# Optimization experiments

Measured on AMD Instinct MI355X. Metric: run time of the kernel, lower is better.

The kernel has to match this reference:

```python
import jax, jax.numpy as jnp
import numpy as np

TEMP = 0.07
EPS = 1e-6
NORM_EPS = 1e-12  # F.normalize default eps
LN_EPS = 1e-5

B, D, H, W = 32, 256, 64, 64
K = 256
DFF = 2048


def _l2norm(v, axis):
    n = jnp.sqrt(jnp.sum(v * v, axis=axis, keepdims=True))
    return v / jnp.maximum(n, NORM_EPS)


def _layernorm(v, g, b):
    mu = jnp.mean(v, axis=-1, keepdims=True)
    var = jnp.mean((v - mu) ** 2, axis=-1, keepdims=True)
    return (v - mu) * jax.lax.rsqrt(var + LN_EPS) * g + b


def setup_inputs() -> dict:
    key = jax.random.key(0)
    ks = jax.random.split(key, 8)
    s1 = 1.0 / np.sqrt(D)
    s2 = 1.0 / np.sqrt(DFF)
    return {
        "x": jax.random.normal(ks[0], (B, D, H, W), jnp.float32),
        "tgt": jax.random.normal(ks[1], (B, K, D), jnp.float32),
        "w1": jax.random.uniform(ks[2], (DFF, D), jnp.float32, -s1, s1),
        "b1": jax.random.uniform(ks[3], (DFF,), jnp.float32, -s1, s1),
        "w2": jax.random.uniform(ks[4], (D, DFF), jnp.float32, -s2, s2),
        "b2": jax.random.uniform(ks[5], (D,), jnp.float32, -s2, s2),
        "g2": jnp.ones((D,), jnp.float32),
        "be2": jnp.zeros((D,), jnp.float32),
        "g3": jnp.ones((D,), jnp.float32),
        "be3": jnp.zeros((D,), jnp.float32),
    }


def reference(x, tgt, w1, b1, w2, b2, g2, be2, g3, be3):
    # slot cross-attention with L2-normalized q/k
    tn = _l2norm(tgt, axis=2)           # (b,k,d)
    xn = _l2norm(x, axis=1)             # (b,d,h,w)
    dots = jnp.einsum('bkd,bdhw->bkhw', tn, xn)
    attn = jax.nn.softmax(dots / TEMP, axis=1) + EPS          # softmax over slots
    attn = attn / jnp.sum(attn, axis=(2, 3), keepdims=True)   # spatial normalization
    tgt2 = jnp.einsum('bdhw,bkhw->bkd', x, attn)
    t = _layernorm(tgt + tgt2, g2, be2)
    # FFN (dropout = identity in eval)
    ff = jnp.maximum(t @ w1.T + b1, 0.0) @ w2.T + b2
    return _layernorm(t + ff, g3, be3)
```

## Files before the change

kernel.cpp:

```cpp
#include <hip/hip_runtime.h>
#include <hip/hip_bf16.h>

using bf16 = __hip_bfloat16;

typedef __attribute__((ext_vector_type(8))) short short8;
typedef __attribute__((ext_vector_type(4))) float f32x4;

constexpr int Bb = 32, Dd = 256, HWw = 4096, Kk = 256, Ff = 2048;
constexpr float TEMP_INV = 1.0f / 0.07f;
constexpr float EPSf = 1e-6f;
constexpr float NORM_EPSf = 1e-12f;
constexpr float LN_EPSf = 1e-5f;
constexpr size_t PKD = (size_t)Bb * Kk * Dd;

static __device__ __forceinline__ float b2f(bf16 v) { return __bfloat162float(v); }
static __device__ __forceinline__ bf16 f2b(float v) { return __float2bfloat16(v); }


__global__ __launch_bounds__(64) void k_tn(const float* __restrict__ tgt,
                                           bf16* __restrict__ tnbf) {
  int row = blockIdx.x;
  int b = row >> 8, slot = row & 255;
  int lane = threadIdx.x;
  const float* src = tgt + (size_t)row * Dd + lane * 4;
  float v[4];
#pragma unroll
  for (int u = 0; u < 4; u++) v[u] = src[u];
  float ss = v[0] * v[0] + v[1] * v[1] + v[2] * v[2] + v[3] * v[3];
#pragma unroll
  for (int m = 32; m >= 1; m >>= 1) ss += __shfl_xor(ss, m, 64);
  float inv = 1.0f / fmaxf(sqrtf(ss), NORM_EPSf);
  bf16 o[4] __attribute__((aligned(8)));
#pragma unroll
  for (int u = 0; u < 4; u++) o[u] = f2b(v[u] * inv);
  int s = lane >> 3;
  int q2 = (lane >> 1) & 3;
  int jh = (lane & 1) * 4;
  size_t fi = (size_t)((slot >> 4) * 64 + q2 * 16 + (slot & 15));
  *(float2*)(tnbf + ((size_t)(b * 8 + s) * 1024 + fi) * 8 + jh) = *(float2*)o;
}

__global__ __launch_bounds__(64) void k_prew1(const float* __restrict__ w1,
                                              bf16* __restrict__ w1bf) {
  int f = blockIdx.x;
  int lane = threadIdx.x;
  const float* src = w1 + (size_t)f * Dd + lane * 4;
  bf16 o[4] __attribute__((aligned(8)));
#pragma unroll
  for (int u = 0; u < 4; u++) o[u] = f2b(src[u]);
  int s = lane >> 3;
  int q2 = (lane >> 1) & 3;
  int jh = (lane & 1) * 4;
  size_t fi = (size_t)(((f & 63) >> 4) * 64 + q2 * 16 + (f & 15));
  *(float2*)(w1bf + ((size_t)((f >> 6) * 8 + s) * 256 + fi) * 8 + jh) = *(float2*)o;
}

__global__ __launch_bounds__(64) void k_prew2(const float* __restrict__ w2,
                                              bf16* __restrict__ w2bf) {
  int d = blockIdx.x;
  int lane = threadIdx.x;
  const float* src = w2 + (size_t)d * Ff + lane * 32;
  size_t gbase = (size_t)((d >> 6) * 64 + lane) * 256;
  int fbase = ((d & 63) >> 4) * 64 + (d & 15);
#pragma unroll
  for (int q2 = 0; q2 < 4; q2++) {
    float4 v0 = *(const float4*)(src + q2 * 8);
    float4 v1 = *(const float4*)(src + q2 * 8 + 4);
    bf16 o[8] __attribute__((aligned(16)));
    o[0] = f2b(v0.x); o[1] = f2b(v0.y); o[2] = f2b(v0.z); o[3] = f2b(v0.w);
    o[4] = f2b(v1.x); o[5] = f2b(v1.y); o[6] = f2b(v1.z); o[7] = f2b(v1.w);
    *(float4*)(w2bf + (gbase + fbase + q2 * 16) * 8) = *(float4*)o;
  }
}

#define MFMA16(a, b, c) __builtin_amdgcn_mfma_f32_16x16x32_bf16(a, b, c, 0, 0, 0)

__global__ __launch_bounds__(256, 3) void k_dots(const bf16* __restrict__ tnbf,
                                                 const float* __restrict__ x,
                                                 bf16* __restrict__ xb_bf,
                                                 bf16* __restrict__ attn_bf,
                                                 float* __restrict__ S) {
  __shared__ __align__(16) char smem[23296];
  bf16* Bs = (bf16*)smem;
  float* ssred = (float*)(smem + 16640);
  float* nxl = (float*)(smem + 20992);
  float* red = (float*)(smem + 21248);
  int b = blockIdx.x >> 6;
  int hw0 = (blockIdx.x & 63) * 64;
  int tid = threadIdx.x;
  int wave = tid >> 6, lane = tid & 63;
  int quad = lane >> 4, nl = lane & 15;

  int dp = tid >> 4;
  int ch = tid & 15;
  int qb = dp >> 2;
  int jb = (dp & 3) * 2;

  f32x4 acc[4][4];
#pragma unroll
  for (int i = 0; i < 4; i++)
#pragma unroll
    for (int j = 0; j < 4; j++) acc[i][j] = (f32x4){0.f, 0.f, 0.f, 0.f};
  float ssp[4] = {0.f, 0.f, 0.f, 0.f};

  int spx = (hw0 >> 5) + (ch >> 3);
  int q2x = (ch >> 1) & 3;
  int jx = (ch & 1) * 4;

  const float* xbase = x + (size_t)((b << 8) + 2 * dp) * HWw + hw0 + ch * 4;
  float4 va4[2], vb4[2];
#pragma unroll
  for (int q = 0; q < 2; q++) {
    const float* xr = xbase + (size_t)(q * 32) * HWw;
    va4[q] = *(const float4*)xr;
    vb4[q] = *(const float4*)(xr + HWw);
  }
  short8 afp[4];
  {
    const bf16* ts0 = tnbf + (size_t)(b * 8) * 1024 * 8;
#pragma unroll
    for (int mt = 0; mt < 4; mt++)
      afp[mt] = *(const short8*)(ts0 + (size_t)(((wave << 2) + mt) * 64 + lane) * 8);
  }

#pragma unroll 1
  for (int p = 0; p < 4; p++) {
    bf16* bsb = Bs + (p & 1) * 2 * 2080;
    bf16 paS[2][4] __attribute__((aligned(8)));
    bf16 pbS[2][4] __attribute__((aligned(8)));
#pragma unroll
    for (int q = 0; q < 2; q++) {
      float vva[4] = {va4[q].x, va4[q].y, va4[q].z, va4[q].w};
      float vvb[4] = {vb4[q].x, vb4[q].y, vb4[q].z, vb4[q].w};
#pragma unroll
      for (int jj = 0; jj < 4; jj++) {
        ssp[jj] += vva[jj] * vva[jj] + vvb[jj] * vvb[jj];
        paS[q][jj] = f2b(vva[jj]);
        pbS[q][jj] = f2b(vvb[jj]);
      }
#pragma unroll
      for (int jj = 0; jj < 4; jj++) {
        int hwl = ch * 4 + jj;
        int nt = hwl >> 4;
        int li = (qb << 4) | (hwl & 15);
        union { bf16 h[2]; unsigned int u; } pk;
        pk.h[0] = paS[q][jj];
        pk.h[1] = pbS[q][jj];
        *(unsigned int*)&bsb[q * 2080 + nt * 520 + li * 8 + jb] = pk.u;
      }
    }
    __syncthreads();

#pragma unroll
    for (int q = 0; q < 2; q++) {
      int s = 2 * p + q;
      int d0r = s * 32 + 2 * dp;
      int fiA = (d0r >> 4) * 64 + q2x * 16 + (d0r & 15);
      size_t base = ((size_t)(b * 128) + spx) * 1024;
      *(float2*)(xb_bf + (base + fiA) * 8 + jx) = *(float2*)paS[q];
      *(float2*)(xb_bf + (base + fiA + 1) * 8 + jx) = *(float2*)pbS[q];
    }
    if (p < 3) {
#pragma unroll
      for (int q = 0; q < 2; q++) {
        const float* xr = xbase + (size_t)(((p + 1) * 2 + q) * 32) * HWw;
        va4[q] = *(const float4*)xr;
        vb4[q] = *(const float4*)(xr + HWw);
      }
    }
#pragma unroll
    for (int q = 0; q < 2; q++) {
      int s = 2 * p + q;
      short8 af[4];
#pragma unroll
      for (int mt = 0; mt < 4; mt++) af[mt] = afp[mt];
      if (s < 7) {
        const bf16* tsrc = tnbf + (size_t)(b * 8 + s + 1) * 1024 * 8;
#pragma unroll
        for (int mt = 0; mt < 4; mt++)
          afp[mt] = *(const short8*)(tsrc + (size_t)(((wave << 2) + mt) * 64 + lane) * 8);
      }
      short8 bfv[4];
#pragma unroll
      for (int nt = 0; nt < 4; nt++)
        bfv[nt] = *(const short8*)(bsb + q * 2080 + nt * 520 + lane * 8);
#pragma unroll
      for (int mt = 0; mt < 4; mt++)
#pragma unroll
        for (int nt = 0; nt < 4; nt++) acc[mt][nt] = MFMA16(af[mt], bfv[nt], acc[mt][nt]);
    }
  }

#pragma unroll
  for (int jj = 0; jj < 4; jj++) ssred[(ch * 4 + jj) * 17 + dp] = ssp[jj];
  __syncthreads();
  if (tid < 64) {
    float sum = 0.f;
#pragma unroll
    for (int i = 0; i < 16; i++) sum += ssred[tid * 17 + i];
    nxl[tid] = TEMP_INV / fmaxf(sqrtf(sum), NORM_EPSf);
  }
  __syncthreads();

  float sc[4];
#pragma unroll
  for (int nt = 0; nt < 4; nt++) sc[nt] = nxl[nt * 16 + nl];
#pragma unroll
  for (int mt = 0; mt < 4; mt++)
#pragma unroll
    for (int nt = 0; nt < 4; nt++)
#pragma unroll
      for (int r = 0; r < 4; r++) acc[mt][nt][r] *= sc[nt];

  float* red2 = red + 256;

  float pmax[4];
#pragma unroll
  for (int nt = 0; nt < 4; nt++) {
    float m = acc[0][nt][0];
#pragma unroll
    for (int mt = 0; mt < 4; mt++)
#pragma unroll
      for (int r = 0; r < 4; r++) m = fmaxf(m, acc[mt][nt][r]);
    m = fmaxf(m, __shfl_xor(m, 16, 64));
    m = fmaxf(m, __shfl_xor(m, 32, 64));
    pmax[nt] = m;
  }
  if (lane < 16) {
#pragma unroll
    for (int nt = 0; nt < 4; nt++) red[((wave << 2) + nt) * 16 + nl] = pmax[nt];
  }
  __syncthreads();
  float cmax[4];
#pragma unroll
  for (int nt = 0; nt < 4; nt++) {
    float m = red[nt * 16 + nl];
#pragma unroll
    for (int w2 = 1; w2 < 4; w2++) m = fmaxf(m, red[((w2 << 2) + nt) * 16 + nl]);
    cmax[nt] = m;
  }

  float psum[4];
#pragma unroll
  for (int nt = 0; nt < 4; nt++) {
    float s = 0.f;
#pragma unroll
    for (int mt = 0; mt < 4; mt++)
#pragma unroll
      for (int r = 0; r < 4; r++) {
        float e = __expf(acc[mt][nt][r] - cmax[nt]);
        acc[mt][nt][r] = e;
        s += e;
      }
    s += __shfl_xor(s, 16, 64);
    s += __shfl_xor(s, 32, 64);
    psum[nt] = s;
  }
  if (lane < 16) {
#pragma unroll
    for (int nt = 0; nt < 4; nt++) red2[((wave << 2) + nt) * 16 + nl] = psum[nt];
  }
  __syncthreads();
  float ci[4];
#pragma unroll
  for (int nt = 0; nt < 4; nt++) {
    float s = 0.f;
#pragma unroll
    for (int w2 = 0; w2 < 4; w2++) s += red2[((w2 << 2) + nt) * 16 + nl];
    ci[nt] = 1.0f / s;
  }

#pragma unroll
  for (int mt = 0; mt < 4; mt++) {
    int slotg = (b << 8) + (wave << 6) + (mt << 4) + (quad << 2);
#pragma unroll
    for (int r = 0; r < 4; r++) {
      float rs = 0.f;
#pragma unroll
      for (int nt = 0; nt < 4; nt++) {
        bf16 hb = f2b(acc[mt][nt][r] * ci[nt] + EPSf);
        float q = b2f(hb);
        acc[mt][nt][r] = q;
        rs += q;
      }
      rs += __shfl_xor(rs, 1, 64);
      rs += __shfl_xor(rs, 2, 64);
      rs += __shfl_xor(rs, 4, 64);
      rs += __shfl_xor(rs, 8, 64);
      if (nl == 0) atomicAdd(&S[slotg + r], rs);
    }
  }

  __syncthreads();
  bf16* rp = (bf16*)smem;
  int jat = nl & 7;
#pragma unroll
  for (int h = 0; h < 2; h++) {
#pragma unroll
    for (int mt = 0; mt < 4; mt++) {
      int fi0 = ((wave << 2) + mt) * 64 + (quad << 2);
#pragma unroll
      for (int ntl = 0; ntl < 2; ntl++) {
        int nt = (h << 1) + ntl;
        int q2p = (ntl << 1) + (nl >> 3);
#pragma unroll
        for (int r = 0; r < 4; r++) {
          int fi = fi0 + q2p * 16 + r;
          int fisw = fi ^ ((fi >> 3) & 3);
          rp[fisw * 8 + jat] = f2b(acc[mt][nt][r]);
        }
      }
    }
    __syncthreads();
    size_t gbase = ((size_t)(b * 128) + (hw0 >> 5) + h) * 1024 * 8;
#pragma unroll
    for (int u = 0; u < 4; u++) {
      int fl = u * 256 + tid;
      int fg = fl ^ ((fl >> 3) & 3);
      short8 vv = *(const short8*)(rp + (size_t)fl * 8);
      *(short8*)(attn_bf + gbase + (size_t)fg * 8) = vv;
    }
    if (h == 0) __syncthreads();
  }
}

__global__ __launch_bounds__(256) void k_gemm2(const bf16* __restrict__ attn_bf,
                                               const bf16* __restrict__ xb_bf,
                                               float* __restrict__ t2p) {
  int n = blockIdx.x;
  int b = n & 31;
  int r2 = n >> 5;
  int kp = r2 & 3;
  int dgrp = (r2 >> 2) & 3;
  int hs = r2 >> 4;
  int tid = threadIdx.x;
  int wave = tid >> 6, lane = tid & 63;
  int wr = wave >> 1, wc = wave & 1;

  f32x4 acc[2][2];
#pragma unroll
  for (int i = 0; i < 2; i++)
#pragma unroll
    for (int j = 0; j < 2; j++) acc[i][j] = (f32x4){0.f, 0.f, 0.f, 0.f};

  const bf16* Abase = attn_bf + ((size_t)(b * 128 + hs * 32) * 1024 + (size_t)(kp * 4 + wr * 2) * 64) * 8;
  const bf16* Bbase = xb_bf + ((size_t)(b * 128 + hs * 32) * 1024 + (size_t)(dgrp * 4 + wc * 2) * 64) * 8;
#pragma unroll 4
  for (int st = 0; st < 32; st++) {
    const bf16* Ap = Abase + (size_t)st * 1024 * 8;
    const bf16* Bp = Bbase + (size_t)st * 1024 * 8;
    short8 a0 = *(const short8*)(Ap + (size_t)lane * 8);
    short8 a1 = *(const short8*)(Ap + (size_t)(64 + lane) * 8);
    short8 b0 = *(const short8*)(Bp + (size_t)lane * 8);
    short8 b1 = *(const short8*)(Bp + (size_t)(64 + lane) * 8);
    acc[0][0] = MFMA16(a0, b0, acc[0][0]);
    acc[0][1] = MFMA16(a0, b1, acc[0][1]);
    acc[1][0] = MFMA16(a1, b0, acc[1][0]);
    acc[1][1] = MFMA16(a1, b1, acc[1][1]);
  }
  float* dst = t2p + (size_t)hs * PKD;
  int quad = lane >> 4, nl = lane & 15;
#pragma unroll
  for (int i = 0; i < 2; i++)
#pragma unroll
    for (int r = 0; r < 4; r++) {
      int row = (b << 8) + kp * 64 + wr * 32 + i * 16 + quad * 4 + r;
#pragma unroll
      for (int j = 0; j < 2; j++) {
        int col = dgrp * 64 + wc * 32 + j * 16 + nl;
        dst[(size_t)row * Dd + col] = acc[i][j][r];
      }
    }
}

__global__ __launch_bounds__(64) void k_ln_pre(const float* __restrict__ t2p,
                                               const float* __restrict__ S,
                                               const float* __restrict__ tgt,
                                               const float* __restrict__ g,
                                               const float* __restrict__ be,
                                               float* __restrict__ t,
                                               bf16* __restrict__ tbf) {
  int row = blockIdx.x;
  int lane = threadIdx.x;
  float sInv = 1.0f / S[row];
  size_t off = (size_t)row * Dd + lane * 4;
  float4 a0 = *(const float4*)(t2p + off);
  float4 a1 = *(const float4*)(t2p + PKD + off);
  float4 a2 = *(const float4*)(t2p + 2 * PKD + off);
  float4 a3 = *(const float4*)(t2p + 3 * PKD + off);
  const float* pt = tgt + off;
  float v[4];
  v[0] = (a0.x + a1.x + a2.x + a3.x) * sInv + pt[0];
  v[1] = (a0.y + a1.y + a2.y + a3.y) * sInv + pt[1];
  v[2] = (a0.z + a1.z + a2.z + a3.z) * sInv + pt[2];
  v[3] = (a0.w + a1.w + a2.w + a3.w) * sInv + pt[3];
  float s1 = v[0] + v[1] + v[2] + v[3];
  float s2 = v[0] * v[0] + v[1] * v[1] + v[2] * v[2] + v[3] * v[3];
#pragma unroll
  for (int m = 32; m >= 1; m >>= 1) {
    s1 += __shfl_xor(s1, m, 64);
    s2 += __shfl_xor(s2, m, 64);
  }
  float mu = s1 * (1.0f / 256.0f);
  float var = s2 * (1.0f / 256.0f) - mu * mu;
  float rs = rsqrtf(fmaxf(var, 0.f) + LN_EPSf);
  float* po = t + (size_t)row * Dd + lane * 4;
  bf16 o[4] __attribute__((aligned(8)));
#pragma unroll
  for (int u = 0; u < 4; u++) {
    float val = (v[u] - mu) * rs * g[lane * 4 + u] + be[lane * 4 + u];
    po[u] = val;
    o[u] = f2b(val);
  }
  int s = lane >> 3;
  int q2 = (lane >> 1) & 3;
  int jh = (lane & 1) * 4;
  size_t fi = (size_t)(((row & 63) >> 4) * 64 + q2 * 16 + (row & 15));
  *(float2*)(tbf + ((size_t)((row >> 6) * 8 + s) * 256 + fi) * 8 + jh) = *(float2*)o;
}

__global__ __launch_bounds__(256) void k_ffn1(const bf16* __restrict__ tbf,
                                              const bf16* __restrict__ w1bf,
                                              const float* __restrict__ b1,
                                              bf16* __restrict__ h1bf) {
  __shared__ __align__(16) bf16 rp[512 * 8];
  int rowgrp = blockIdx.x >> 5;
  int fgrp = blockIdx.x & 31;
  int tid = threadIdx.x;
  int wave = tid >> 6, lane = tid & 63;
  int am = (wave >> 1) * 2, bn = (wave & 1) * 2;

  f32x4 acc[2][2];
#pragma unroll
  for (int i = 0; i < 2; i++)
#pragma unroll
    for (int j = 0; j < 2; j++) acc[i][j] = (f32x4){0.f, 0.f, 0.f, 0.f};

  const bf16* Abase = tbf + (size_t)rowgrp * 8 * 256 * 8;
  const bf16* Bbase = w1bf + (size_t)fgrp * 8 * 256 * 8;
#pragma unroll
  for (int s = 0; s < 8; s++) {
    short8 af[2], bfr[2];
#pragma unroll
    for (int i = 0; i < 2; i++)
      af[i] = *(const short8*)(Abase + ((size_t)s * 256 + ((am + i) * 64 + lane)) * 8);
#pragma unroll
    for (int j = 0; j < 2; j++)
      bfr[j] = *(const short8*)(Bbase + ((size_t)s * 256 + ((bn + j) * 64 + lane)) * 8);
#pragma unroll
    for (int i = 0; i < 2; i++)
#pragma unroll
      for (int j = 0; j < 2; j++) acc[i][j] = MFMA16(af[i], bfr[j], acc[i][j]);
  }
  int quad = lane >> 4, nl = lane & 15;
  int jat = nl & 7;
#pragma unroll
  for (int j = 0; j < 2; j++) {
    int f = fgrp * 64 + (bn + j) * 16 + nl;
    float bias = b1[f];
    int seth = (bn + j) >> 1;
    int q2p = ((bn + j) & 1) * 2 + (nl >> 3);
#pragma unroll
    for (int i = 0; i < 2; i++) {
      int fiBase = (am + i) * 64 + q2p * 16 + (quad << 2);
#pragma unroll
      for (int r = 0; r < 4; r++) {
        float val = fmaxf(acc[i][j][r] + bias, 0.f);
        int fi = fiBase + r;
        int fisw = fi ^ ((fi >> 3) & 3);
        rp[(seth * 256 + fisw) * 8 + jat] = f2b(val);
      }
    }
  }
  __syncthreads();
  size_t sp0 = (size_t)(rowgrp * 64) + fgrp * 2;
#pragma unroll
  for (int u = 0; u < 2; u++) {
    int loc = tid;
    int fg = loc ^ ((loc >> 3) & 3);
    short8 vv = *(const short8*)(rp + ((size_t)u * 256 + loc) * 8);
    *(short8*)(h1bf + ((sp0 + u) * 256 + fg) * 8) = vv;
  }
}

__global__ __launch_bounds__(256) void k_ffn2(const bf16* __restrict__ h1bf,
                                              const bf16* __restrict__ w2bf,
                                              float* __restrict__ o2) {
  __shared__ float redsm[4 * 4160];
  int n = blockIdx.x;
  int rowgrp = n >> 2;
  int cg = n & 3;
  int tid = threadIdx.x;
  int wave = tid >> 6, lane = tid & 63;

  f32x4 acc[4][4];
#pragma unroll
  for (int i = 0; i < 4; i++)
#pragma unroll
    for (int j = 0; j < 4; j++) acc[i][j] = (f32x4){0.f, 0.f, 0.f, 0.f};

#pragma unroll 4
  for (int stl = 0; stl < 16; stl++) {
    int sg = wave * 16 + stl;
    const bf16* Ab = h1bf + ((size_t)(rowgrp * 64 + sg) * 256) * 8;
    const bf16* Bbv = w2bf + ((size_t)(cg * 64 + sg) * 256) * 8;
    short8 af[4], bfr[4];
#pragma unroll
    for (int mt = 0; mt < 4; mt++)
      af[mt] = *(const short8*)(Ab + (size_t)(mt * 64 + lane) * 8);
#pragma unroll
    for (int nt = 0; nt < 4; nt++)
      bfr[nt] = *(const short8*)(Bbv + (size_t)(nt * 64 + lane) * 8);
#pragma unroll
    for (int mt = 0; mt < 4; mt++)
#pragma unroll
      for (int nt = 0; nt < 4; nt++) acc[mt][nt] = MFMA16(af[mt], bfr[nt], acc[mt][nt]);
  }
  int quad = lane >> 4, nl = lane & 15;
  float* my = redsm + wave * 4160;
#pragma unroll
  for (int mt = 0; mt < 4; mt++)
#pragma unroll
    for (int r = 0; r < 4; r++) {
      int row = mt * 16 + quad * 4 + r;
#pragma unroll
      for (int nt = 0; nt < 4; nt++)
        my[row * 65 + nt * 16 + nl] = acc[mt][nt][r];
    }
  __syncthreads();
#pragma unroll
  for (int u = 0; u < 16; u++) {
    int o = u * 256 + tid;
    int row = o >> 6, col = o & 63;
    int li = row * 65 + col;
    float ssum = redsm[li] + redsm[4160 + li] + redsm[8320 + li] + redsm[12480 + li];
    o2[(size_t)(rowgrp * 64 + row) * Dd + cg * 64 + col] = ssum;
  }
}

__global__ __launch_bounds__(64) void k_ln_out(const float* __restrict__ o2,
                                               const float* __restrict__ b2v,
                                               const float* __restrict__ t,
                                               const float* __restrict__ g,
                                               const float* __restrict__ be,
                                               float* __restrict__ out) {
  int row = blockIdx.x;
  int lane = threadIdx.x;
  size_t off = (size_t)row * Dd + lane * 4;
  float4 aq = *(const float4*)(o2 + off);
  const float* pt = t + off;
  float v[4];
  v[0] = aq.x + b2v[lane * 4 + 0] + pt[0];
  v[1] = aq.y + b2v[lane * 4 + 1] + pt[1];
  v[2] = aq.z + b2v[lane * 4 + 2] + pt[2];
  v[3] = aq.w + b2v[lane * 4 + 3] + pt[3];
  float s1 = v[0] + v[1] + v[2] + v[3];
  float s2 = v[0] * v[0] + v[1] * v[1] + v[2] * v[2] + v[3] * v[3];
#pragma unroll
  for (int m = 32; m >= 1; m >>= 1) {
    s1 += __shfl_xor(s1, m, 64);
    s2 += __shfl_xor(s2, m, 64);
  }
  float mu = s1 * (1.0f / 256.0f);
  float var = s2 * (1.0f / 256.0f) - mu * mu;
  float rs = rsqrtf(fmaxf(var, 0.f) + LN_EPSf);
  float* pw = out + (size_t)row * Dd + lane * 4;
#pragma unroll
  for (int u = 0; u < 4; u++)
    pw[u] = (v[u] - mu) * rs * g[lane * 4 + u] + be[lane * 4 + u];
}

extern "C" void kernel_launch(void* const* d_in, const int* in_sizes, int n_in,
                              void* d_out, int out_size, void* d_ws, size_t ws_size,
                              hipStream_t stream) {
  const float* x = (const float*)d_in[0];
  const float* tgt = (const float*)d_in[1];
  const float* w1 = (const float*)d_in[2];
  const float* b1 = (const float*)d_in[3];
  const float* w2 = (const float*)d_in[4];
  const float* b2v = (const float*)d_in[5];
  const float* g2 = (const float*)d_in[6];
  const float* be2 = (const float*)d_in[7];
  const float* g3 = (const float*)d_in[8];
  const float* be3 = (const float*)d_in[9];
  float* out = (float*)d_out;

  char* w = (char*)d_ws;
  bf16* tnbf = (bf16*)w;     w += (size_t)Bb * Kk * Dd * 2;
  float* S = (float*)w;      w += (size_t)Bb * Kk * 4;
  float* t = (float*)w;      w += (size_t)Bb * Kk * Dd * 4;
  bf16* attn_bf = (bf16*)w;  w += (size_t)Bb * HWw * Kk * 2;
  bf16* h1bf = (bf16*)w;     w += (size_t)Bb * Kk * Ff * 2;
  bf16* xb_bf = (bf16*)w;    w += (size_t)Bb * Dd * HWw * 2;

  bf16* tbf = tnbf;
  bf16* w1bf = attn_bf;
  bf16* w2bf = attn_bf + (size_t)Ff * Dd;
  float* t2p = (float*)h1bf;
  float* o2 = (float*)xb_bf;

  hipMemsetAsync(S, 0, (size_t)Bb * Kk * 4, stream);
  k_tn<<<Bb * Kk, 64, 0, stream>>>(tgt, tnbf);
  k_dots<<<Bb * (HWw / 64), 256, 0, stream>>>(tnbf, x, xb_bf, attn_bf, S);
  k_gemm2<<<2048, 256, 0, stream>>>(attn_bf, xb_bf, t2p);
  k_prew1<<<Ff, 64, 0, stream>>>(w1, w1bf);
  k_prew2<<<Dd, 64, 0, stream>>>(w2, w2bf);
  k_ln_pre<<<Bb * Kk, 64, 0, stream>>>(t2p, S, tgt, g2, be2, t, tbf);
  k_ffn1<<<(Bb * Kk / 64) * (Ff / 64), 256, 0, stream>>>(tbf, w1bf, b1, h1bf);
  k_ffn2<<<512, 256, 0, stream>>>(h1bf, w2bf, o2);
  k_ln_out<<<Bb * Kk, 64, 0, stream>>>(o2, b2v, t, g3, be3, out);
}
```

Baseline: 392.3 us.

## Fuse FFN GEMMs into one kernel keeping hidden activations in shared memory

Merges the two FFN GEMM kernels into one kernel in which each 512-thread block handles 32 token rows. Each block computes 64-wide chunks of the ReLU hidden layer into a double-buffered LDS tile and immediately multiplies them by W2. This removes the global write and read of the bf16 hidden activations (32x256x2048) and one launch. It also merges the two weight-conversion kernels into one launch. The cost is fewer blocks (256), per-chunk barriers, and W2 being re-read from global memory by every block.

```diff
diff --git a/kernel.cpp b/kernel.cpp
--- a/kernel.cpp
+++ b/kernel.cpp
@@ -40,36 +40,37 @@
   *(float2*)(tnbf + ((size_t)(b * 8 + s) * 1024 + fi) * 8 + jh) = *(float2*)o;
 }
 
-__global__ __launch_bounds__(64) void k_prew1(const float* __restrict__ w1,
-                                              bf16* __restrict__ w1bf) {
-  int f = blockIdx.x;
+__global__ __launch_bounds__(64) void k_prew(const float* __restrict__ w1,
+                                             const float* __restrict__ w2,
+                                             bf16* __restrict__ w1bf,
+                                             bf16* __restrict__ w2bf) {
+  int bidx = blockIdx.x;
   int lane = threadIdx.x;
-  const float* src = w1 + (size_t)f * Dd + lane * 4;
-  bf16 o[4] __attribute__((aligned(8)));
-#pragma unroll
-  for (int u = 0; u < 4; u++) o[u] = f2b(src[u]);
-  int s = lane >> 3;
-  int q2 = (lane >> 1) & 3;
-  int jh = (lane & 1) * 4;
-  size_t fi = (size_t)(((f & 63) >> 4) * 64 + q2 * 16 + (f & 15));
-  *(float2*)(w1bf + ((size_t)((f >> 6) * 8 + s) * 256 + fi) * 8 + jh) = *(float2*)o;
-}
-
-__global__ __launch_bounds__(64) void k_prew2(const float* __restrict__ w2,
-                                              bf16* __restrict__ w2bf) {
-  int d = blockIdx.x;
-  int lane = threadIdx.x;
-  const float* src = w2 + (size_t)d * Ff + lane * 32;
-  size_t gbase = (size_t)((d >> 6) * 64 + lane) * 256;
-  int fbase = ((d & 63) >> 4) * 64 + (d & 15);
-#pragma unroll
-  for (int q2 = 0; q2 < 4; q2++) {
-    float4 v0 = *(const float4*)(src + q2 * 8);
-    float4 v1 = *(const float4*)(src + q2 * 8 + 4);
-    bf16 o[8] __attribute__((aligned(16)));
-    o[0] = f2b(v0.x); o[1] = f2b(v0.y); o[2] = f2b(v0.z); o[3] = f2b(v0.w);
-    o[4] = f2b(v1.x); o[5] = f2b(v1.y); o[6] = f2b(v1.z); o[7] = f2b(v1.w);
-    *(float4*)(w2bf + (gbase + fbase + q2 * 16) * 8) = *(float4*)o;
+  if (bidx < Ff) {
+    int f = bidx;
+    const float* src = w1 + (size_t)f * Dd + lane * 4;
+    bf16 o[4] __attribute__((aligned(8)));
+#pragma unroll
+    for (int u = 0; u < 4; u++) o[u] = f2b(src[u]);
+    int s = lane >> 3;
+    int q2 = (lane >> 1) & 3;
+    int jh = (lane & 1) * 4;
+    size_t fi = (size_t)(((f & 63) >> 4) * 64 + q2 * 16 + (f & 15));
+    *(float2*)(w1bf + ((size_t)((f >> 6) * 8 + s) * 256 + fi) * 8 + jh) = *(float2*)o;
+  } else {
+    int d = bidx - Ff;
+    const float* src = w2 + (size_t)d * Ff + lane * 32;
+    size_t gbase = (size_t)((d >> 6) * 64 + lane) * 256;
+    int fbase = ((d & 63) >> 4) * 64 + (d & 15);
+#pragma unroll
+    for (int q2 = 0; q2 < 4; q2++) {
+      float4 v0 = *(const float4*)(src + q2 * 8);
+      float4 v1 = *(const float4*)(src + q2 * 8 + 4);
+      bf16 o[8] __attribute__((aligned(16)));
+      o[0] = f2b(v0.x); o[1] = f2b(v0.y); o[2] = f2b(v0.z); o[3] = f2b(v0.w);
+      o[4] = f2b(v1.x); o[5] = f2b(v1.y); o[6] = f2b(v1.z); o[7] = f2b(v1.w);
+      *(float4*)(w2bf + (gbase + fbase + q2 * 16) * 8) = *(float4*)o;
+    }
   }
 }
 
@@ -419,123 +420,98 @@
   *(float2*)(tbf + ((size_t)((row >> 6) * 8 + s) * 256 + fi) * 8 + jh) = *(float2*)o;
 }
 
-__global__ __launch_bounds__(256) void k_ffn1(const bf16* __restrict__ tbf,
-                                              const bf16* __restrict__ w1bf,
-                                              const float* __restrict__ b1,
-                                              bf16* __restrict__ h1bf) {
-  __shared__ __align__(16) bf16 rp[512 * 8];
-  int rowgrp = blockIdx.x >> 5;
-  int fgrp = blockIdx.x & 31;
+__global__ __launch_bounds__(512, 2) void k_ffn(const bf16* __restrict__ tbf,
+                                                const bf16* __restrict__ w1bf,
+                                                const float* __restrict__ b1,
+                                                const bf16* __restrict__ w2bf,
+                                                float* __restrict__ o2) {
+  __shared__ __align__(16) bf16 rp[2][2 * 128 * 8];
+  int rg = blockIdx.x;
   int tid = threadIdx.x;
   int wave = tid >> 6, lane = tid & 63;
-  int am = (wave >> 1) * 2, bn = (wave & 1) * 2;
-
-  f32x4 acc[2][2];
+  int quad = lane >> 4, nl = lane & 15;
+  int mh = wave >> 2, fq = wave & 3;
+  int gg = rg >> 1, half = rg & 1;
+
+  short8 af1[8];
+  {
+    const bf16* Ab = tbf + ((size_t)(gg * 8) * 256 + (size_t)((half * 2 + mh) * 64 + lane)) * 8;
+#pragma unroll
+    for (int s = 0; s < 8; s++) af1[s] = *(const short8*)(Ab + (size_t)s * 2048);
+  }
+
+  f32x4 acc2[2][2];
 #pragma unroll
   for (int i = 0; i < 2; i++)
 #pragma unroll
-    for (int j = 0; j < 2; j++) acc[i][j] = (f32x4){0.f, 0.f, 0.f, 0.f};
-
-  const bf16* Abase = tbf + (size_t)rowgrp * 8 * 256 * 8;
-  const bf16* Bbase = w1bf + (size_t)fgrp * 8 * 256 * 8;
-#pragma unroll
-  for (int s = 0; s < 8; s++) {
-    short8 af[2], bfr[2];
-#pragma unroll
-    for (int i = 0; i < 2; i++)
-      af[i] = *(const short8*)(Abase + ((size_t)s * 256 + ((am + i) * 64 + lane)) * 8);
-#pragma unroll
-    for (int j = 0; j < 2; j++)
-      bfr[j] = *(const short8*)(Bbase + ((size_t)s * 256 + ((bn + j) * 64 + lane)) * 8);
-#pragma unroll
-    for (int i = 0; i < 2; i++)
-#pragma unroll
-      for (int j = 0; j < 2; j++) acc[i][j] = MFMA16(af[i], bfr[j], acc[i][j]);
-  }
-  int quad = lane >> 4, nl = lane & 15;
-  int jat = nl & 7;
-#pragma unroll
-  for (int j = 0; j < 2; j++) {
-    int f = fgrp * 64 + (bn + j) * 16 + nl;
-    float bias = b1[f];
-    int seth = (bn + j) >> 1;
-    int q2p = ((bn + j) & 1) * 2 + (nl >> 3);
-#pragma unroll
-    for (int i = 0; i < 2; i++) {
-      int fiBase = (am + i) * 64 + q2p * 16 + (quad << 2);
-#pragma unroll
-      for (int r = 0; r < 4; r++) {
-        float val = fmaxf(acc[i][j][r] + bias, 0.f);
-        int fi = fiBase + r;
+    for (int j = 0; j < 2; j++) acc2[i][j] = (f32x4){0.f, 0.f, 0.f, 0.f};
+
+  int setw = fq >> 1;
+  int q2w = (fq * 2 + (nl >> 3)) & 3;
+  int jw = nl & 7;
+  int dgrp2 = wave >> 1;
+  int ntp0 = (wave & 1) * 2;
+
+  auto G1 = [&](int cn) {
+    f32x4 a1a = (f32x4){0.f, 0.f, 0.f, 0.f};
+    f32x4 a1b = (f32x4){0.f, 0.f, 0.f, 0.f};
+    const bf16* Bb1 = w1bf + ((size_t)(cn * 8) * 256 + (size_t)(fq * 64 + lane)) * 8;
+#pragma unroll
+    for (int s = 0; s < 8; s += 2) {
+      short8 bv0 = *(const short8*)(Bb1 + (size_t)s * 2048);
+      short8 bv1 = *(const short8*)(Bb1 + (size_t)(s + 1) * 2048);
+      a1a = MFMA16(af1[s], bv0, a1a);
+      a1b = MFMA16(af1[s + 1], bv1, a1b);
+    }
+    float bias = b1[cn * 64 + fq * 16 + nl];
+    bf16* rpw = &rp[cn & 1][0];
+#pragma unroll
+    for (int r = 0; r < 4; r++) {
+      float hv = fmaxf(a1a[r] + a1b[r] + bias, 0.f);
+      int fi = mh * 64 + q2w * 16 + quad * 4 + r;
+      int fisw = fi ^ ((fi >> 3) & 3);
+      rpw[(setw * 128 + fisw) * 8 + jw] = f2b(hv);
+    }
+  };
+
+  G1(0);
+  __syncthreads();
+
+#pragma unroll 1
+  for (int c = 0; c < 32; c++) {
+    if (c < 31) G1(c + 1);
+    const bf16* rpr = &rp[c & 1][0];
+#pragma unroll
+    for (int ks = 0; ks < 2; ks++) {
+      short8 a2[2];
+#pragma unroll
+      for (int mi = 0; mi < 2; mi++) {
+        int fi = mi * 64 + lane;
         int fisw = fi ^ ((fi >> 3) & 3);
-        rp[(seth * 256 + fisw) * 8 + jat] = f2b(val);
-      }
-    }
-  }
-  __syncthreads();
-  size_t sp0 = (size_t)(rowgrp * 64) + fgrp * 2;
-#pragma unroll
-  for (int u = 0; u < 2; u++) {
-    int loc = tid;
-    int fg = loc ^ ((loc >> 3) & 3);
-    short8 vv = *(const short8*)(rp + ((size_t)u * 256 + loc) * 8);
-    *(short8*)(h1bf + ((sp0 + u) * 256 + fg) * 8) = vv;
-  }
-}
-
-__global__ __launch_bounds__(256) void k_ffn2(const bf16* __restrict__ h1bf,
-                                              const bf16* __restrict__ w2bf,
-                                              float* __restrict__ o2) {
-  __shared__ float redsm[4 * 4160];
-  int n = blockIdx.x;
-  int rowgrp = n >> 2;
-  int cg = n & 3;
-  int tid = threadIdx.x;
-  int wave = tid >> 6, lane = tid & 63;
-
-  f32x4 acc[4][4];
-#pragma unroll
-  for (int i = 0; i < 4; i++)
-#pragma unroll
-    for (int j = 0; j < 4; j++) acc[i][j] = (f32x4){0.f, 0.f, 0.f, 0.f};
-
-#pragma unroll 4
-  for (int stl = 0; stl < 16; stl++) {
-    int sg = wave * 16 + stl;
-    const bf16* Ab = h1bf + ((size_t)(rowgrp * 64 + sg) * 256) * 8;
-    const bf16* Bbv = w2bf + ((size_t)(cg * 64 + sg) * 256) * 8;
-    short8 af[4], bfr[4];
-#pragma unroll
-    for (int mt = 0; mt < 4; mt++)
-      af[mt] = *(const short8*)(Ab + (size_t)(mt * 64 + lane) * 8);
-#pragma unroll
-    for (int nt = 0; nt < 4; nt++)
-      bfr[nt] = *(const short8*)(Bbv + (size_t)(nt * 64 + lane) * 8);
-#pragma unroll
-    for (int mt = 0; mt < 4; mt++)
-#pragma unroll
-      for (int nt = 0; nt < 4; nt++) acc[mt][nt] = MFMA16(af[mt], bfr[nt], acc[mt][nt]);
-  }
-  int quad = lane >> 4, nl = lane & 15;
-  float* my = redsm + wave * 4160;
-#pragma unroll
-  for (int mt = 0; mt < 4; mt++)
+        a2[mi] = *(const short8*)(rpr + (ks * 128 + fisw) * 8);
+      }
+      int sg = c * 2 + ks;
+#pragma unroll
+      for (int nt = 0; nt < 2; nt++) {
+        short8 b2 = *(const short8*)(w2bf + ((size_t)(dgrp2 * 64 + sg) * 256 + (size_t)((ntp0 + nt) * 64 + lane)) * 8);
+        acc2[0][nt] = MFMA16(a2[0], b2, acc2[0][nt]);
+        acc2[1][nt] = MFMA16(a2[1], b2, acc2[1][nt]);
+      }
+    }
+    __syncthreads();
+  }
+
+#pragma unroll
+  for (int mi = 0; mi < 2; mi++)
 #pragma unroll
     for (int r = 0; r < 4; r++) {
-      int row = mt * 16 + quad * 4 + r;
-#pragma unroll
-      for (int nt = 0; nt < 4; nt++)
-        my[row * 65 + nt * 16 + nl] = acc[mt][nt][r];
-    }
-  __syncthreads();
-#pragma unroll
-  for (int u = 0; u < 16; u++) {
-    int o = u * 256 + tid;
-    int row = o >> 6, col = o & 63;
-    int li = row * 65 + col;
-    float ssum = redsm[li] + redsm[4160 + li] + redsm[8320 + li] + redsm[12480 + li];
-    o2[(size_t)(rowgrp * 64 + row) * Dd + cg * 64 + col] = ssum;
-  }
+      int row = rg * 32 + mi * 16 + quad * 4 + r;
+#pragma unroll
+      for (int nt = 0; nt < 2; nt++) {
+        int col = wave * 32 + nt * 16 + nl;
+        o2[(size_t)row * Dd + col] = acc2[mi][nt][r];
+      }
+    }
 }
 
 __global__ __launch_bounds__(64) void k_ln_out(const float* __restrict__ o2,
@@ -590,23 +566,21 @@
   float* S = (float*)w;      w += (size_t)Bb * Kk * 4;
   float* t = (float*)w;      w += (size_t)Bb * Kk * Dd * 4;
   bf16* attn_bf = (bf16*)w;  w += (size_t)Bb * HWw * Kk * 2;
-  bf16* h1bf = (bf16*)w;     w += (size_t)Bb * Kk * Ff * 2;
+  bf16* h1reg = (bf16*)w;    w += (size_t)Bb * Kk * Ff * 2;
   bf16* xb_bf = (bf16*)w;    w += (size_t)Bb * Dd * HWw * 2;
 
   bf16* tbf = tnbf;
   bf16* w1bf = attn_bf;
   bf16* w2bf = attn_bf + (size_t)Ff * Dd;
-  float* t2p = (float*)h1bf;
+  float* t2p = (float*)h1reg;
   float* o2 = (float*)xb_bf;
 
   hipMemsetAsync(S, 0, (size_t)Bb * Kk * 4, stream);
   k_tn<<<Bb * Kk, 64, 0, stream>>>(tgt, tnbf);
   k_dots<<<Bb * (HWw / 64), 256, 0, stream>>>(tnbf, x, xb_bf, attn_bf, S);
   k_gemm2<<<2048, 256, 0, stream>>>(attn_bf, xb_bf, t2p);
-  k_prew1<<<Ff, 64, 0, stream>>>(w1, w1bf);
-  k_prew2<<<Dd, 64, 0, stream>>>(w2, w2bf);
+  k_prew<<<Ff + Dd, 64, 0, stream>>>(w1, w2, w1bf, w2bf);
   k_ln_pre<<<Bb * Kk, 64, 0, stream>>>(t2p, S, tgt, g2, be2, t, tbf);
-  k_ffn1<<<(Bb * Kk / 64) * (Ff / 64), 256, 0, stream>>>(tbf, w1bf, b1, h1bf);
-  k_ffn2<<<512, 256, 0, stream>>>(h1bf, w2bf, o2);
+  k_ffn<<<(Bb * Kk) / 32, 512, 0, stream>>>(tbf, w1bf, b1, w2bf, o2);
   k_ln_out<<<Bb * Kk, 64, 0, stream>>>(o2, b2v, t, g3, be3, out);
 }
```

New measurement: 392.2 us (median of 2 runs). About the same (-0.0%).
